# Performance work log

Hardware: AMD Instinct MI355X
Metric: run time of the kernel (lower is better)

Reference implementation:

```python
import jax, jax.numpy as jnp
import numpy as np

STRIDES = (8, 16, 32)
FEAT_SIZES = ((80, 80), (40, 40), (20, 20))  # (h, w) per level for 640x640 input
OFFSET = 0.5
NMS_K = 300
IOU_THR = 0.65
EPS = 1e-7


def make_priors():
    """MlvlPointGenerator.grid_priors with with_stride=True, flattened over levels."""
    pts, strs = [], []
    for (h, w), s in zip(FEAT_SIZES, STRIDES):
        xs = (jnp.arange(w, dtype=jnp.float32) + OFFSET) * s
        ys = (jnp.arange(h, dtype=jnp.float32) + OFFSET) * s
        yy, xx = jnp.meshgrid(ys, xs, indexing='ij')
        pts.append(jnp.stack([xx.reshape(-1), yy.reshape(-1)], -1))
        strs.append(jnp.full((h * w, 2), float(s), dtype=jnp.float32))
    return jnp.concatenate(pts, 0), jnp.concatenate(strs, 0)  # [N,2], [N,2]


def pairwise_iou(boxes):  # boxes [K,4] xyxy
    area = jnp.clip(boxes[:, 2] - boxes[:, 0], 0) * jnp.clip(boxes[:, 3] - boxes[:, 1], 0)
    lt = jnp.maximum(boxes[:, None, :2], boxes[None, :, :2])
    rb = jnp.minimum(boxes[:, None, 2:], boxes[None, :, 2:])
    wh = jnp.clip(rb - lt, 0)
    inter = wh[..., 0] * wh[..., 1]
    union = area[:, None] + area[None, :] - inter
    return inter / (union + EPS)


def nms_keep(boxes):  # boxes [K,4] sorted by descending score -> bool keep mask [K]
    K = boxes.shape[0]
    iou = pairwise_iou(boxes)
    idx = jnp.arange(K)

    def body(i, keep):
        sup = (iou[i] > IOU_THR) & (idx > i) & keep[i]
        return keep & ~sup

    return jax.lax.fori_loop(0, K, body, jnp.ones((K,), dtype=bool))


def setup_inputs() -> dict:
    key = jax.random.key(0)
    k1, k2, k3, k4, k5 = jax.random.split(key, 5)
    B, N, K = 128, 8400, 17
    return {
        'cls_scores': jax.random.normal(k1, (B, N, 1), jnp.float32),
        'bbox_preds': jax.random.normal(k2, (B, N, 4), jnp.float32),
        'objectness': jax.random.normal(k3, (B, N), jnp.float32),
        'kpt_offsets': jax.random.normal(k4, (B, N, K, 2), jnp.float32),
        'kpt_vis_preds': jax.random.normal(k5, (B, N, K), jnp.float32),
    }


def reference(cls_scores, bbox_preds, objectness, kpt_offsets, kpt_vis_preds):
    priors, strides = make_priors()  # [N,2] each
    # bbox decode: center-offset + exp wh, YOLOX style
    xy = bbox_preds[..., :2] * strides + priors            # [B,N,2]
    wh = jnp.exp(bbox_preds[..., 2:4]) * strides           # [B,N,2]
    boxes = jnp.concatenate([xy - wh * 0.5, xy + wh * 0.5], -1)  # [B,N,4]
    scores = jax.nn.sigmoid(cls_scores[..., 0]) * jax.nn.sigmoid(objectness)  # [B,N]
    # keypoint decode
    kpts = kpt_offsets * strides[:, None, :] + priors[:, None, :]  # [B,N,K,2]
    B, N, K, _ = kpts.shape
    kpts_flat = kpts.reshape(B, N, K * 2)
    vis = jax.nn.sigmoid(kpt_vis_preds)                    # [B,N,K]
    # fixed-size top-k pre-NMS selection
    top_vals, top_idx = jax.lax.top_k(scores, NMS_K)       # [B,NMS_K]
    gather = lambda x: jnp.take_along_axis(x, top_idx[..., None], axis=1)
    boxes_k = gather(boxes)       # [B,NMS_K,4]
    kpts_k = gather(kpts_flat)    # [B,NMS_K,2K]
    vis_k = gather(vis)           # [B,NMS_K,K]
    keep = jax.vmap(nms_keep)(boxes_k)                      # [B,NMS_K] bool
    final_scores = top_vals * keep.astype(top_vals.dtype)
    # [B, NMS_K, 4 + 1 + 2K + K]
    return jnp.concatenate([boxes_k, final_scores[..., None], kpts_k, vis_k], -1)
```

## Files before the change

### kernel.cpp

```cpp
#include <hip/hip_runtime.h>
#include <math.h>

#define BATCH 128
#define NANCH 8400
#define NMSK  300
#define KPT   17
#define OUTC  56
#define CAND  768
#define NBLKE 7650

__device__ __forceinline__ void prior_of(int i, float& stride, float& cx, float& cy) {
    int row, col;
    if (i < 6400)      { stride = 8.0f;  row = i / 80;              col = i - row * 80; }
    else if (i < 8000) { int ii = i - 6400; stride = 16.0f; row = ii / 40; col = ii - row * 40; }
    else               { int ii = i - 8000; stride = 32.0f; row = ii / 20; col = ii - row * 20; }
    cx = ((float)col + 0.5f) * stride;
    cy = ((float)row + 0.5f) * stride;
}

__global__ __launch_bounds__(256) void scores_kernel(
    const float* __restrict__ cls, const float* __restrict__ obj,
    unsigned int* __restrict__ sc)
{
    int i = blockIdx.x * 256 + threadIdx.x;
    if (i < BATCH * NANCH) {
        float ea = (float)exp(-(double)cls[i]);
        float eo = (float)exp(-(double)obj[i]);
        float sa = 1.0f / (1.0f + ea);
        float so = 1.0f / (1.0f + eo);
        sc[i] = __float_as_uint(sa * so);
    }
}

__global__ __launch_bounds__(256) void topk_kernel(
    const float* __restrict__ cls, const float* __restrict__ obj,
    const unsigned int* __restrict__ sc_g, int has_sc,
    int* __restrict__ top_idx, float* __restrict__ top_val)
{
    const int b = blockIdx.x;
    const int tid = threadIdx.x;

    __shared__ unsigned int sc[NANCH];
    __shared__ unsigned int hist[256];
    __shared__ unsigned int suf[256];
    __shared__ unsigned int sh_prefix, sh_k, sh_cnt;
    __shared__ unsigned long long ckey[CAND];

    if (has_sc) {
        const unsigned int* s = sc_g + (size_t)b * NANCH;
        for (int i = tid; i < NANCH; i += 256) sc[i] = s[i];
    } else {
        const float* c = cls + (size_t)b * NANCH;
        const float* o = obj + (size_t)b * NANCH;
        for (int i = tid; i < NANCH; i += 256) {
            float ea = (float)exp(-(double)c[i]);
            float eo = (float)exp(-(double)o[i]);
            sc[i] = __float_as_uint((1.0f / (1.0f + ea)) * (1.0f / (1.0f + eo)));
        }
    }
    if (tid == 0) { sh_prefix = 0u; sh_k = NMSK; sh_cnt = 0u; }
    __syncthreads();

    for (int r = 3; r >= 0; --r) {
        hist[tid] = 0u;
        __syncthreads();
        unsigned int pfx  = sh_prefix;
        unsigned int kcur = sh_k;
        for (int i = tid; i < NANCH; i += 256) {
            unsigned int key = sc[i];
            bool match = (r == 3) || ((key >> ((r + 1) * 8)) == pfx);
            if (match) atomicAdd(&hist[(key >> (r * 8)) & 0xFFu], 1u);
        }
        __syncthreads();
        suf[tid] = hist[tid];
        __syncthreads();
        for (int d = 1; d < 256; d <<= 1) {
            unsigned int v   = suf[tid];
            unsigned int add = (tid + d < 256) ? suf[tid + d] : 0u;
            __syncthreads();
            suf[tid] = v + add;
            __syncthreads();
        }
        unsigned int ge     = suf[tid];
        unsigned int genext = (tid < 255) ? suf[tid + 1] : 0u;
        if (ge >= kcur && genext < kcur) {
            sh_prefix = (pfx << 8) | (unsigned int)tid;
            sh_k      = kcur - genext;
        }
        __syncthreads();
    }

    unsigned int pivot_bits = sh_prefix;
    for (int i = tid; i < NANCH; i += 256) {
        unsigned int key = sc[i];
        if (key >= pivot_bits) {
            unsigned int p = atomicAdd(&sh_cnt, 1u);
            if (p < CAND)
                ckey[p] = ((unsigned long long)key << 32)
                        | (unsigned long long)(0xFFFFFFFFu - (unsigned int)i);
        }
    }
    __syncthreads();
    unsigned int M = sh_cnt; if (M > CAND) M = CAND;

    for (unsigned int j = tid; j < M; j += 256) {
        unsigned long long mine = ckey[j];
        int rank = 0;
        for (unsigned int t2 = 0; t2 < M; ++t2) rank += (ckey[t2] > mine) ? 1 : 0;
        if (rank < NMSK) {
            top_idx[b * NMSK + rank] = (int)(0xFFFFFFFFu - (unsigned int)(mine & 0xFFFFFFFFull));
            top_val[b * NMSK + rank] = __uint_as_float((unsigned int)(mine >> 32));
        }
    }
}

__global__ __launch_bounds__(256) void fused_out_kernel(
    const float* __restrict__ bbox, const float* __restrict__ kofs,
    const float* __restrict__ kvis, const int* __restrict__ top_idx,
    const float* __restrict__ top_val, float* __restrict__ out)
{
    const int tid = threadIdx.x;

    __shared__ float bx1[NMSK], by1[NMSK], bx2[NMSK], by2[NMSK], area[NMSK];
    __shared__ float sval[NMSK];
    __shared__ unsigned long long sup[NMSK][5];
    __shared__ unsigned long long keepw[5];

    if (blockIdx.x < NBLKE) {
        int t  = blockIdx.x * 256 + tid;
        int ci = t % 51;
        int rj = t / 51;
        int j  = rj % NMSK;
        int b  = rj / NMSK;
        int i  = top_idx[b * NMSK + j];
        float stride, cx, cy;
        prior_of(i, stride, cx, cy);
        float v;
        if (ci < 34) {
            float off = kofs[((size_t)b * NANCH + (size_t)i) * 34 + ci];
            v = off * stride + ((ci & 1) ? cy : cx);
        } else {
            float x = kvis[((size_t)b * NANCH + (size_t)i) * KPT + (ci - 34)];
            v = 1.0f / (1.0f + expf(-x));
        }
        out[((size_t)b * NMSK + j) * OUTC + 5 + ci] = v;
        return;
    }

    const int b = blockIdx.x - NBLKE;

    for (int j = tid; j < NMSK; j += 256) {
        int i = top_idx[b * NMSK + j];
        sval[j] = top_val[b * NMSK + j];
        float stride, cx, cy;
        prior_of(i, stride, cx, cy);
        const float* bp = bbox + ((size_t)b * NANCH + (size_t)i) * 4;
        float4 bb = *(const float4*)bp;
        float x = bb.x * stride + cx;
        float y = bb.y * stride + cy;
        float w = expf(bb.z) * stride;
        float h = expf(bb.w) * stride;
        float x1 = x - 0.5f * w, y1 = y - 0.5f * h;
        float x2 = x + 0.5f * w, y2 = y + 0.5f * h;
        bx1[j] = x1; by1[j] = y1; bx2[j] = x2; by2[j] = y2;
        area[j] = fmaxf(x2 - x1, 0.0f) * fmaxf(y2 - y1, 0.0f);
    }
    __syncthreads();

    for (int i = tid; i < NMSK; i += 256) {
        unsigned long long m0 = 0, m1 = 0, m2 = 0, m3 = 0, m4 = 0;
        float ax1 = bx1[i], ay1 = by1[i], ax2 = bx2[i], ay2 = by2[i], aa = area[i];
        for (int j = i + 1; j < NMSK; ++j) {
            float lx = fmaxf(ax1, bx1[j]);
            float ly = fmaxf(ay1, by1[j]);
            float rx = fminf(ax2, bx2[j]);
            float ry = fminf(ay2, by2[j]);
            float iw = fmaxf(rx - lx, 0.0f);
            float ih = fmaxf(ry - ly, 0.0f);
            float inter = iw * ih;
            float iou = inter / (aa + area[j] - inter + 1e-7f);
            if (iou > 0.65f) {
                unsigned long long bit = 1ull << (j & 63);
                switch (j >> 6) {
                    case 0: m0 |= bit; break;
                    case 1: m1 |= bit; break;
                    case 2: m2 |= bit; break;
                    case 3: m3 |= bit; break;
                    default: m4 |= bit; break;
                }
            }
        }
        sup[i][0] = m0; sup[i][1] = m1; sup[i][2] = m2; sup[i][3] = m3; sup[i][4] = m4;
    }
    __syncthreads();

    if (tid < 64) {
        unsigned long long kw;
        if (tid < 4)       kw = ~0ull;
        else if (tid == 4) kw = (1ull << (NMSK - 256)) - 1ull;
        else               kw = 0ull;
        for (int i = 0; i < NMSK; ++i) {
            unsigned int lo = (unsigned int)kw;
            unsigned int hi = (unsigned int)(kw >> 32);
            lo = (unsigned int)__shfl((int)lo, i >> 6, 64);
            hi = (unsigned int)__shfl((int)hi, i >> 6, 64);
            unsigned long long ow = ((unsigned long long)hi << 32) | lo;
            if ((ow >> (i & 63)) & 1ull) {
                if (tid < 5) kw &= ~sup[i][tid];
            }
        }
        if (tid < 5) keepw[tid] = kw;
    }
    __syncthreads();

    float* ob = out + (size_t)b * NMSK * OUTC;
    for (int t = tid; t < NMSK * 5; t += 256) {
        int j  = t / 5;
        int ci = t - j * 5;
        float v;
        if (ci == 0)      v = bx1[j];
        else if (ci == 1) v = by1[j];
        else if (ci == 2) v = bx2[j];
        else if (ci == 3) v = by2[j];
        else {
            bool kp = (keepw[j >> 6] >> (j & 63)) & 1ull;
            v = kp ? sval[j] : 0.0f;
        }
        ob[j * OUTC + ci] = v;
    }
}

extern "C" void kernel_launch(void* const* d_in, const int* in_sizes, int n_in,
                              void* d_out, int out_size, void* d_ws, size_t ws_size,
                              hipStream_t stream) {
    const float* cls  = (const float*)d_in[0];
    const float* bbox = (const float*)d_in[1];
    const float* obj  = (const float*)d_in[2];
    const float* kofs = (const float*)d_in[3];
    const float* kvis = (const float*)d_in[4];
    float* out = (float*)d_out;

    size_t need_idx = (size_t)BATCH * NMSK * sizeof(int);
    size_t need_val = (size_t)BATCH * NMSK * sizeof(float);
    size_t need_sc  = (size_t)BATCH * NANCH * sizeof(unsigned int);

    int*   top_idx = (int*)d_ws;
    float* top_val = (float*)((char*)d_ws + need_idx);
    unsigned int* sc = (unsigned int*)((char*)d_ws + need_idx + need_val);

    int has_sc = (ws_size >= need_idx + need_val + need_sc) ? 1 : 0;

    if (has_sc) {
        int nblk = (BATCH * NANCH + 255) / 256;
        scores_kernel<<<nblk, 256, 0, stream>>>(cls, obj, sc);
    }
    topk_kernel<<<BATCH, 256, 0, stream>>>(cls, obj, sc, has_sc, top_idx, top_val);
    fused_out_kernel<<<NBLKE + BATCH, 256, 0, stream>>>(bbox, kofs, kvis, top_idx, top_val, out);
}
```

Before: 349.3 us.

## Fuse top-k, NMS and output gather into one 1024-thread per-batch kernel

Merges the top-k selection kernel and the output/NMS kernel into a single kernel with one 1024-thread block per batch, so top indices and values stay in shared memory instead of going through global workspace. The suffix scan is replaced with a wavefront shuffle scan, the IoU mask build is split into 64-column word tasks for more parallelism, and the serial NMS sweep runs on one wave while the other waves gather keypoints concurrently. The trade-off is that keypoint gathering, previously spread over about 7650 blocks, now runs in only 128 blocks, which may leave much of the GPU idle during the memory-bound gather.

New measurement: 287.5 us. -17.7%, faster.

```diff
diff --git a/kernel.cpp b/kernel.cpp
--- a/kernel.cpp
+++ b/kernel.cpp
@@ -7,7 +7,7 @@
 #define KPT   17
 #define OUTC  56
 #define CAND  768
-#define NBLKE 7650
+#define NTHR  1024
 
 __device__ __forceinline__ void prior_of(int i, float& stride, float& cx, float& cy) {
     int row, col;
@@ -32,10 +32,11 @@
     }
 }
 
-__global__ __launch_bounds__(256) void topk_kernel(
+__global__ __launch_bounds__(NTHR) void fused_kernel(
     const float* __restrict__ cls, const float* __restrict__ obj,
     const unsigned int* __restrict__ sc_g, int has_sc,
-    int* __restrict__ top_idx, float* __restrict__ top_val)
+    const float* __restrict__ bbox, const float* __restrict__ kofs,
+    const float* __restrict__ kvis, float* __restrict__ out)
 {
     const int b = blockIdx.x;
     const int tid = threadIdx.x;
@@ -45,14 +46,19 @@
     __shared__ unsigned int suf[256];
     __shared__ unsigned int sh_prefix, sh_k, sh_cnt;
     __shared__ unsigned long long ckey[CAND];
+    __shared__ float bx1[NMSK], by1[NMSK], bx2[NMSK], by2[NMSK], area[NMSK];
+    __shared__ float sval[NMSK], pst[NMSK], ppx[NMSK], ppy[NMSK];
+    __shared__ int   sidx[NMSK];
+    __shared__ unsigned long long supl[NMSK * 6];
+    __shared__ unsigned long long keepw[5];
 
     if (has_sc) {
         const unsigned int* s = sc_g + (size_t)b * NANCH;
-        for (int i = tid; i < NANCH; i += 256) sc[i] = s[i];
+        for (int i = tid; i < NANCH; i += NTHR) sc[i] = s[i];
     } else {
         const float* c = cls + (size_t)b * NANCH;
         const float* o = obj + (size_t)b * NANCH;
-        for (int i = tid; i < NANCH; i += 256) {
+        for (int i = tid; i < NANCH; i += NTHR) {
             float ea = (float)exp(-(double)c[i]);
             float eo = (float)exp(-(double)o[i]);
             sc[i] = __float_as_uint((1.0f / (1.0f + ea)) * (1.0f / (1.0f + eo)));
@@ -62,36 +68,47 @@
     __syncthreads();
 
     for (int r = 3; r >= 0; --r) {
-        hist[tid] = 0u;
+        if (tid < 256) hist[tid] = 0u;
         __syncthreads();
         unsigned int pfx  = sh_prefix;
         unsigned int kcur = sh_k;
-        for (int i = tid; i < NANCH; i += 256) {
+        for (int i = tid; i < NANCH; i += NTHR) {
             unsigned int key = sc[i];
             bool match = (r == 3) || ((key >> ((r + 1) * 8)) == pfx);
             if (match) atomicAdd(&hist[(key >> (r * 8)) & 0xFFu], 1u);
         }
         __syncthreads();
-        suf[tid] = hist[tid];
-        __syncthreads();
-        for (int d = 1; d < 256; d <<= 1) {
-            unsigned int v   = suf[tid];
-            unsigned int add = (tid + d < 256) ? suf[tid + d] : 0u;
-            __syncthreads();
-            suf[tid] = v + add;
-            __syncthreads();
-        }
-        unsigned int ge     = suf[tid];
-        unsigned int genext = (tid < 255) ? suf[tid + 1] : 0u;
-        if (ge >= kcur && genext < kcur) {
-            sh_prefix = (pfx << 8) | (unsigned int)tid;
-            sh_k      = kcur - genext;
+        if (tid < 64) {
+            int l = tid;
+            unsigned int b0 = hist[4 * l + 0], b1 = hist[4 * l + 1];
+            unsigned int b2 = hist[4 * l + 2], b3 = hist[4 * l + 3];
+            unsigned int tot = b0 + b1 + b2 + b3;
+            unsigned int v = tot;
+            #pragma unroll
+            for (int d = 1; d < 64; d <<= 1) {
+                unsigned int t2 = (unsigned int)__shfl_down((int)v, d, 64);
+                if (l + d < 64) v += t2;
+            }
+            unsigned int above = v - tot;
+            suf[4 * l + 3] = above + b3;
+            suf[4 * l + 2] = above + b3 + b2;
+            suf[4 * l + 1] = above + b3 + b2 + b1;
+            suf[4 * l + 0] = above + tot;
+        }
+        __syncthreads();
+        if (tid < 256) {
+            unsigned int ge     = suf[tid];
+            unsigned int genext = (tid < 255) ? suf[tid + 1] : 0u;
+            if (ge >= kcur && genext < kcur) {
+                sh_prefix = (pfx << 8) | (unsigned int)tid;
+                sh_k      = kcur - genext;
+            }
         }
         __syncthreads();
     }
 
     unsigned int pivot_bits = sh_prefix;
-    for (int i = tid; i < NANCH; i += 256) {
+    for (int i = tid; i < NANCH; i += NTHR) {
         unsigned int key = sc[i];
         if (key >= pivot_bits) {
             unsigned int p = atomicAdd(&sh_cnt, 1u);
@@ -103,59 +120,24 @@
     __syncthreads();
     unsigned int M = sh_cnt; if (M > CAND) M = CAND;
 
-    for (unsigned int j = tid; j < M; j += 256) {
-        unsigned long long mine = ckey[j];
+    if (tid < (int)M) {
+        unsigned long long mine = ckey[tid];
         int rank = 0;
         for (unsigned int t2 = 0; t2 < M; ++t2) rank += (ckey[t2] > mine) ? 1 : 0;
         if (rank < NMSK) {
-            top_idx[b * NMSK + rank] = (int)(0xFFFFFFFFu - (unsigned int)(mine & 0xFFFFFFFFull));
-            top_val[b * NMSK + rank] = __uint_as_float((unsigned int)(mine >> 32));
-        }
-    }
-}
-
-__global__ __launch_bounds__(256) void fused_out_kernel(
-    const float* __restrict__ bbox, const float* __restrict__ kofs,
-    const float* __restrict__ kvis, const int* __restrict__ top_idx,
-    const float* __restrict__ top_val, float* __restrict__ out)
-{
-    const int tid = threadIdx.x;
-
-    __shared__ float bx1[NMSK], by1[NMSK], bx2[NMSK], by2[NMSK], area[NMSK];
-    __shared__ float sval[NMSK];
-    __shared__ unsigned long long sup[NMSK][5];
-    __shared__ unsigned long long keepw[5];
-
-    if (blockIdx.x < NBLKE) {
-        int t  = blockIdx.x * 256 + tid;
-        int ci = t % 51;
-        int rj = t / 51;
-        int j  = rj % NMSK;
-        int b  = rj / NMSK;
-        int i  = top_idx[b * NMSK + j];
+            sidx[rank] = (int)(0xFFFFFFFFu - (unsigned int)(mine & 0xFFFFFFFFull));
+            sval[rank] = __uint_as_float((unsigned int)(mine >> 32));
+        }
+    }
+    __syncthreads();
+
+    if (tid < NMSK) {
+        int j = tid;
+        int i = sidx[j];
         float stride, cx, cy;
         prior_of(i, stride, cx, cy);
-        float v;
-        if (ci < 34) {
-            float off = kofs[((size_t)b * NANCH + (size_t)i) * 34 + ci];
-            v = off * stride + ((ci & 1) ? cy : cx);
-        } else {
-            float x = kvis[((size_t)b * NANCH + (size_t)i) * KPT + (ci - 34)];
-            v = 1.0f / (1.0f + expf(-x));
-        }
-        out[((size_t)b * NMSK + j) * OUTC + 5 + ci] = v;
-        return;
-    }
-
-    const int b = blockIdx.x - NBLKE;
-
-    for (int j = tid; j < NMSK; j += 256) {
-        int i = top_idx[b * NMSK + j];
-        sval[j] = top_val[b * NMSK + j];
-        float stride, cx, cy;
-        prior_of(i, stride, cx, cy);
-        const float* bp = bbox + ((size_t)b * NANCH + (size_t)i) * 4;
-        float4 bb = *(const float4*)bp;
+        pst[j] = stride; ppx[j] = cx; ppy[j] = cy;
+        float4 bb = *(const float4*)(bbox + ((size_t)b * NANCH + (size_t)i) * 4);
         float x = bb.x * stride + cx;
         float y = bb.y * stride + cy;
         float w = expf(bb.z) * stride;
@@ -167,10 +149,14 @@
     }
     __syncthreads();
 
-    for (int i = tid; i < NMSK; i += 256) {
-        unsigned long long m0 = 0, m1 = 0, m2 = 0, m3 = 0, m4 = 0;
+    for (int t = tid; t < NMSK * 5; t += NTHR) {
+        int w = t / NMSK;
+        int i = t - w * NMSK;
+        int jlo = w * 64; if (jlo < i + 1) jlo = i + 1;
+        int jhi = w * 64 + 64; if (jhi > NMSK) jhi = NMSK;
+        unsigned long long m = 0;
         float ax1 = bx1[i], ay1 = by1[i], ax2 = bx2[i], ay2 = by2[i], aa = area[i];
-        for (int j = i + 1; j < NMSK; ++j) {
+        for (int j = jlo; j < jhi; ++j) {
             float lx = fmaxf(ax1, bx1[j]);
             float ly = fmaxf(ay1, by1[j]);
             float rx = fminf(ax2, bx2[j]);
@@ -179,42 +165,50 @@
             float ih = fmaxf(ry - ly, 0.0f);
             float inter = iw * ih;
             float iou = inter / (aa + area[j] - inter + 1e-7f);
-            if (iou > 0.65f) {
-                unsigned long long bit = 1ull << (j & 63);
-                switch (j >> 6) {
-                    case 0: m0 |= bit; break;
-                    case 1: m1 |= bit; break;
-                    case 2: m2 |= bit; break;
-                    case 3: m3 |= bit; break;
-                    default: m4 |= bit; break;
-                }
+            if (iou > 0.65f) m |= 1ull << (j & 63);
+        }
+        supl[i * 6 + w] = m;
+    }
+    __syncthreads();
+
+    if (tid < 64) {
+        unsigned long long k0 = ~0ull, k1 = ~0ull, k2 = ~0ull, k3 = ~0ull;
+        unsigned long long k4 = (1ull << (NMSK - 256)) - 1ull;
+        const unsigned long long* sp = supl;
+        #define GSTEP(KW, I) \
+            if (((KW) >> ((I) & 63)) & 1ull) { \
+                const unsigned long long* s = sp + (size_t)(I) * 6; \
+                k0 &= ~s[0]; k1 &= ~s[1]; k2 &= ~s[2]; k3 &= ~s[3]; k4 &= ~s[4]; }
+        for (int i = 0;   i < 64;   ++i) { GSTEP(k0, i) }
+        for (int i = 64;  i < 128;  ++i) { GSTEP(k1, i) }
+        for (int i = 128; i < 192;  ++i) { GSTEP(k2, i) }
+        for (int i = 192; i < 256;  ++i) { GSTEP(k3, i) }
+        for (int i = 256; i < NMSK; ++i) { GSTEP(k4, i) }
+        #undef GSTEP
+        if (tid == 0) { keepw[0] = k0; keepw[1] = k1; keepw[2] = k2; keepw[3] = k3; keepw[4] = k4; }
+    } else {
+        const float* kof = kofs + (size_t)b * NANCH * 34;
+        const float* kvi = kvis + (size_t)b * NANCH * KPT;
+        float* ob = out + (size_t)b * NMSK * OUTC;
+        for (int e = tid - 64; e < NMSK * 51; e += NTHR - 64) {
+            int j  = e / 51;
+            int ci = e - j * 51;
+            int i  = sidx[j];
+            float v;
+            if (ci < 34) {
+                float off = kof[(size_t)i * 34 + ci];
+                v = off * pst[j] + ((ci & 1) ? ppy[j] : ppx[j]);
+            } else {
+                float x = kvi[(size_t)i * KPT + (ci - 34)];
+                v = 1.0f / (1.0f + expf(-x));
             }
-        }
-        sup[i][0] = m0; sup[i][1] = m1; sup[i][2] = m2; sup[i][3] = m3; sup[i][4] = m4;
-    }
-    __syncthreads();
-
-    if (tid < 64) {
-        unsigned long long kw;
-        if (tid < 4)       kw = ~0ull;
-        else if (tid == 4) kw = (1ull << (NMSK - 256)) - 1ull;
-        else               kw = 0ull;
-        for (int i = 0; i < NMSK; ++i) {
-            unsigned int lo = (unsigned int)kw;
-            unsigned int hi = (unsigned int)(kw >> 32);
-            lo = (unsigned int)__shfl((int)lo, i >> 6, 64);
-            hi = (unsigned int)__shfl((int)hi, i >> 6, 64);
-            unsigned long long ow = ((unsigned long long)hi << 32) | lo;
-            if ((ow >> (i & 63)) & 1ull) {
-                if (tid < 5) kw &= ~sup[i][tid];
-            }
-        }
-        if (tid < 5) keepw[tid] = kw;
+            ob[j * OUTC + 5 + ci] = v;
+        }
     }
     __syncthreads();
 
     float* ob = out + (size_t)b * NMSK * OUTC;
-    for (int t = tid; t < NMSK * 5; t += 256) {
+    for (int t = tid; t < NMSK * 5; t += NTHR) {
         int j  = t / 5;
         int ci = t - j * 5;
         float v;
@@ -240,20 +234,14 @@
     const float* kvis = (const float*)d_in[4];
     float* out = (float*)d_out;
 
-    size_t need_idx = (size_t)BATCH * NMSK * sizeof(int);
-    size_t need_val = (size_t)BATCH * NMSK * sizeof(float);
-    size_t need_sc  = (size_t)BATCH * NANCH * sizeof(unsigned int);
-
-    int*   top_idx = (int*)d_ws;
-    float* top_val = (float*)((char*)d_ws + need_idx);
-    unsigned int* sc = (unsigned int*)((char*)d_ws + need_idx + need_val);
-
-    int has_sc = (ws_size >= need_idx + need_val + need_sc) ? 1 : 0;
+    size_t need_sc = (size_t)BATCH * NANCH * sizeof(unsigned int);
+    unsigned int* sc = (unsigned int*)d_ws;
+    int has_sc = (ws_size >= need_sc) ? 1 : 0;
 
     if (has_sc) {
         int nblk = (BATCH * NANCH + 255) / 256;
         scores_kernel<<<nblk, 256, 0, stream>>>(cls, obj, sc);
     }
-    topk_kernel<<<BATCH, 256, 0, stream>>>(cls, obj, sc, has_sc, top_idx, top_val);
-    fused_out_kernel<<<NBLKE + BATCH, 256, 0, stream>>>(bbox, kofs, kvis, top_idx, top_val, out);
-}
+    fused_kernel<<<BATCH, NTHR, 0, stream>>>(cls, obj, sc, has_sc,
+                                             bbox, kofs, kvis, out);
+}
```
